# Optimization experiments

Measured on AMD Instinct MI355X. Metric: run time of the kernel, lower is better.

## Reference

```python
import jax, jax.numpy as jnp
import numpy as np
from jax import lax

B, C = 16, 80
LEVELS = [(100, 128), (50, 64), (25, 32), (13, 16), (7, 8)]
STRIDES = [8, 16, 32, 64, 128]
SCORE_THR = 0.05
IOU_THR = 0.6
MAX_DET = 1000


def make_coords(h, w, stride):
    # FCOS: center of each cell in original-image coordinates, order (x, y)
    ys = jnp.arange(h, dtype=jnp.float32) * stride + stride // 2
    xs = jnp.arange(w, dtype=jnp.float32) * stride + stride // 2
    yy, xx = jnp.meshgrid(ys, xs, indexing='ij')
    return jnp.stack([xx.reshape(-1), yy.reshape(-1)], axis=-1)  # [h*w, 2]


def flatten_levels(feats):
    # list of [B, c, h, w] -> [B, sum(h*w), c]
    return jnp.concatenate(
        [f.transpose(0, 2, 3, 1).reshape(f.shape[0], -1, f.shape[1]) for f in feats], axis=1)


def pairwise_iou(boxes):
    # boxes [N,4]; +1 area convention, matching the torch box_nms
    x1, y1, x2, y2 = boxes[:, 0], boxes[:, 1], boxes[:, 2], boxes[:, 3]
    areas = (x2 - x1 + 1.0) * (y2 - y1 + 1.0)
    xmin = jnp.maximum(x1[:, None], x1[None, :])
    ymin = jnp.maximum(y1[:, None], y1[None, :])
    xmax = jnp.minimum(x2[:, None], x2[None, :])
    ymax = jnp.minimum(y2[:, None], y2[None, :])
    inter = jnp.clip(xmax - xmin, 0.0) * jnp.clip(ymax - ymin, 0.0)
    return inter / (areas[:, None] + areas[None, :] - inter)


def nms_keep_mask(boxes, valid, thr):
    # boxes are sorted by descending score (top_k sorted=True) -> greedy order = index order
    n = boxes.shape[0]
    iou = pairwise_iou(boxes)
    idx = jnp.arange(n)

    def body(i, sup):
        kept = jnp.logical_not(sup[i])
        return sup | (kept & (iou[i] > thr) & (idx > i))

    sup = lax.fori_loop(0, n, body, jnp.logical_not(valid))
    return valid & jnp.logical_not(sup)


def detect_forward(cls_feats, ctr_feats, reg_feats):
    cls_logits = flatten_levels(cls_feats)   # [B, P, C]
    ctr_logits = flatten_levels(ctr_feats)   # [B, P, 1]
    reg_preds = flatten_levels(reg_feats)    # [B, P, 4] (l, t, r, b)
    coords = jnp.concatenate(
        [make_coords(h, w, s) for (h, w), s in zip(LEVELS, STRIDES)], axis=0)  # [P, 2]

    cls_preds = jax.nn.sigmoid(cls_logits)
    ctr_preds = jax.nn.sigmoid(ctr_logits)[..., 0]
    cls_scores = jnp.max(cls_preds, axis=-1) * ctr_preds        # add_centerness=True
    cls_classes = jnp.argmax(cls_preds, axis=-1) + 1            # [B, P] int

    boxes = jnp.concatenate(
        [coords[None] - reg_preds[..., :2], coords[None] + reg_preds[..., 2:]], axis=-1)

    max_num = min(MAX_DET, cls_scores.shape[-1])
    scores_topk, topk_ind = lax.top_k(cls_scores, max_num)      # sorted descending
    classes_topk = jnp.take_along_axis(cls_classes, topk_ind, axis=1)
    boxes_topk = jnp.take_along_axis(boxes, topk_ind[..., None], axis=1)

    valid = scores_topk >= SCORE_THR
    # batched_nms class-offset trick
    max_coord = jnp.max(boxes_topk, axis=(1, 2), keepdims=True)
    offs = classes_topk.astype(boxes_topk.dtype)[..., None] * (max_coord + 1.0)
    boxes_for_nms = boxes_topk + offs

    keep = jax.vmap(lambda b, v: nms_keep_mask(b, v, IOU_THR))(boxes_for_nms, valid)
    keep_f = keep.astype(scores_topk.dtype)
    # fixed-shape masked outputs (torch version returns ragged per-batch lists)
    return scores_topk * keep_f, classes_topk * keep, boxes_topk * keep_f[..., None]


def setup_inputs() -> dict:
    key = jax.random.key(0)
    ks = jax.random.split(key, 3 * len(LEVELS))
    inp = {}
    for i, (h, w) in enumerate(LEVELS):
        inp[f'cls{i}'] = jax.random.normal(ks[3 * i], (B, C, h, w), jnp.float32)
        inp[f'ctr{i}'] = jax.random.normal(ks[3 * i + 1], (B, 1, h, w), jnp.float32)
        # positive ltrb offsets of plausible magnitude
        inp[f'reg{i}'] = jax.random.uniform(ks[3 * i + 2], (B, 4, h, w), jnp.float32) * 64.0 + 1.0
    return inp


def reference(cls0, cls1, cls2, cls3, cls4, ctr0, ctr1, ctr2, ctr3, ctr4,
              reg0, reg1, reg2, reg3, reg4):
    return detect_forward([cls0, cls1, cls2, cls3, cls4],
                          [ctr0, ctr1, ctr2, ctr3, ctr4],
                          [reg0, reg1, reg2, reg3, reg4])
```

## Files before the change

### kernel.cpp

```cpp
#include <hip/hip_runtime.h>
#include <stdint.h>

#define NANCH 17064
#define BATCH 16
#define NCLS 80
#define KDET 1000
#define SCORE_THR 0.05f
#define IOU_THR 0.6f

typedef unsigned long long u64;
typedef unsigned int u32;

__device__ __forceinline__ float sigf(float x) { return 1.0f / (1.0f + expf(-x)); }

__device__ __forceinline__ void decode_anchor(int n, int& l, int& h, int& w) {
  if (n < 12800)      { l = 0; h = n >> 7;               w = n & 127; }
  else if (n < 16000) { l = 1; int r = n - 12800; h = r >> 6; w = r & 63; }
  else if (n < 16800) { l = 2; int r = n - 16000; h = r >> 5; w = r & 31; }
  else if (n < 17008) { l = 3; int r = n - 16800; h = r >> 4; w = r & 15; }
  else                { l = 4; int r = n - 17008; h = r >> 3; w = r & 7; }
}

__global__ __launch_bounds__(256) void k_score(
    const float* __restrict__ cls0, const float* __restrict__ ctr0,
    const float* __restrict__ cls1, const float* __restrict__ ctr1,
    const float* __restrict__ cls2, const float* __restrict__ ctr2,
    const float* __restrict__ cls3, const float* __restrict__ ctr3,
    const float* __restrict__ cls4, const float* __restrict__ ctr4,
    u32* __restrict__ sb, unsigned char* __restrict__ cl8)
{
  int n = blockIdx.x * blockDim.x + threadIdx.x;
  if (n >= NANCH) return;
  int b = blockIdx.y;
  int l, h, w; decode_anchor(n, l, h, w);
  const float* cp; const float* tp; int H, W;
  switch (l) {
    case 0: cp = cls0; tp = ctr0; H = 100; W = 128; break;
    case 1: cp = cls1; tp = ctr1; H = 50;  W = 64;  break;
    case 2: cp = cls2; tp = ctr2; H = 25;  W = 32;  break;
    case 3: cp = cls3; tp = ctr3; H = 13;  W = 16;  break;
    default: cp = cls4; tp = ctr4; H = 7;  W = 8;   break;
  }
  int hw = H * W;
  const float* base = cp + (size_t)b * NCLS * hw + h * W + w;
  float ms = -1.0f; int am = 0;
  for (int c = 0; c < NCLS; ++c) {
    float s = sigf(base[(size_t)c * hw]);
    if (s > ms) { ms = s; am = c; }
  }
  float ct = sigf(tp[(size_t)b * hw + h * W + w]);
  float score = ms * ct;
  sb[b * NANCH + n] = __float_as_uint(score);
  cl8[b * NANCH + n] = (unsigned char)am;
}

__global__ __launch_bounds__(1024) void k_topk(
    const float* __restrict__ reg0, const float* __restrict__ reg1,
    const float* __restrict__ reg2, const float* __restrict__ reg3,
    const float* __restrict__ reg4,
    const u32* __restrict__ sb, const unsigned char* __restrict__ cl8,
    float4* __restrict__ nbxG, float* __restrict__ areaG,
    float* __restrict__ scoreG, int* __restrict__ clsG, float4* __restrict__ boxG)
{
  __shared__ u32 hist[1024];
  __shared__ u32 wtot[16];
  __shared__ float wmaxS[16];
  __shared__ u64 keys[2048];
  __shared__ int s_T1, s_above, s_T2, s_cnt;

  const int tid = threadIdx.x;
  const int b = blockIdx.x;
  const int lane = tid & 63, wv = tid >> 6;
  const u32* sbb = sb + b * NANCH;

  hist[tid] = 0;
  __syncthreads();
  for (int n = tid; n < NANCH; n += 1024) atomicAdd(&hist[sbb[n] >> 22], 1u);
  __syncthreads();
  u32 h = hist[tid];
  u32 s = h;
  for (int d = 1; d < 64; d <<= 1) { u32 y = (u32)__shfl_down((int)s, d); if (lane + d < 64) s += y; }
  if (lane == 0) wtot[wv] = s;
  hist[tid] = 0;
  __syncthreads();
  {
    u32 add = 0;
    for (int w2 = wv + 1; w2 < 16; ++w2) add += wtot[w2];
    s += add;
  }
  if (s >= (u32)KDET && s - h < (u32)KDET) { s_T1 = tid; s_above = (int)(s - h); }
  __syncthreads();
  const int T1 = s_T1; const int above = s_above;

  for (int n = tid; n < NANCH; n += 1024) {
    u32 bits = sbb[n];
    if ((int)(bits >> 22) == T1) atomicAdd(&hist[(bits >> 12) & 1023u], 1u);
  }
  __syncthreads();
  h = hist[tid];
  s = h;
  for (int d = 1; d < 64; d <<= 1) { u32 y = (u32)__shfl_down((int)s, d); if (lane + d < 64) s += y; }
  if (lane == 0) wtot[wv] = s;
  __syncthreads();
  {
    u32 add = 0;
    for (int w2 = wv + 1; w2 < 16; ++w2) add += wtot[w2];
    s += add;
  }
  if (above + (int)s >= KDET && above + (int)(s - h) < KDET) s_T2 = tid;
  if (tid == 0) s_cnt = 0;
  __syncthreads();
  const int T2 = s_T2;

  for (int n = tid; n < NANCH; n += 1024) {
    u32 bits = sbb[n];
    int c1 = (int)(bits >> 22);
    bool cand = (c1 > T1) || (c1 == T1 && (int)((bits >> 12) & 1023u) >= T2);
    if (cand) {
      int pos = atomicAdd(&s_cnt, 1);
      if (pos < 2048) keys[pos] = ((u64)bits << 32) | (u64)(u32)(~(u32)n);
    }
  }
  __syncthreads();
  int C = s_cnt; if (C > 2048) C = 2048;

  float mymax = -3.4e38f;
  int posA = -1, clA = 0; float scA = 0; float4 boxA = make_float4(0, 0, 0, 0);
  int posB = -1, clB = 0; float scB = 0; float4 boxB = make_float4(0, 0, 0, 0);
  for (int t = tid; t < C; t += 1024) {
    u64 key = keys[t];
    int cnt = 0;
    for (int ss = 0; ss < C; ++ss) cnt += (keys[ss] > key) ? 1 : 0;
    if (cnt < KDET) {
      u32 bits = (u32)(key >> 32);
      int n = (int)(~(u32)(key & 0xFFFFFFFFull));
      float score = __uint_as_float(bits);
      int clsv = (int)cl8[b * NANCH + n] + 1;
      int l, hh, ww; decode_anchor(n, l, hh, ww);
      const float* rp; int W, ST, HF;
      switch (l) {
        case 0: rp = reg0; W = 128; ST = 8;   HF = 4;  break;
        case 1: rp = reg1; W = 64;  ST = 16;  HF = 8;  break;
        case 2: rp = reg2; W = 32;  ST = 32;  HF = 16; break;
        case 3: rp = reg3; W = 16;  ST = 64;  HF = 32; break;
        default: rp = reg4; W = 8;  ST = 128; HF = 64; break;
      }
      int hw; switch (l) { case 0: hw = 12800; break; case 1: hw = 3200; break;
                           case 2: hw = 800; break; case 3: hw = 208; break; default: hw = 56; }
      float cx = (float)(ww * ST + HF);
      float cy = (float)(hh * ST + HF);
      const float* rb = rp + (size_t)b * 4 * hw + hh * W + ww;
      float r0 = rb[0], r1 = rb[hw], r2 = rb[2 * hw], r3 = rb[3 * hw];
      float4 bx = make_float4(cx - r0, cy - r1, cx + r2, cy + r3);
      mymax = fmaxf(mymax, fmaxf(fmaxf(bx.x, bx.y), fmaxf(bx.z, bx.w)));
      if (posA < 0) { posA = cnt; scA = score; clA = clsv; boxA = bx; }
      else          { posB = cnt; scB = score; clB = clsv; boxB = bx; }
    }
  }

  {
    float wm = mymax;
    for (int d = 1; d < 64; d <<= 1) { float y = __shfl_down(wm, d); if (lane + d < 64) wm = fmaxf(wm, y); }
    if (lane == 0) wmaxS[wv] = wm;
  }
  __syncthreads();
  float maxc = -3.4e38f;
  for (int w2 = 0; w2 < 16; ++w2) maxc = fmaxf(maxc, wmaxS[w2]);

  if (posA >= 0) {
    int o = b * KDET + posA;
    scoreG[o] = scA; clsG[o] = clA; boxG[o] = boxA;
    float off = (float)clA * (maxc + 1.0f);
    float x1 = boxA.x + off, y1 = boxA.y + off, x2 = boxA.z + off, y2 = boxA.w + off;
    nbxG[o] = make_float4(x1, y1, x2, y2);
    areaG[o] = (x2 - x1 + 1.0f) * (y2 - y1 + 1.0f);
  }
  if (posB >= 0) {
    int o = b * KDET + posB;
    scoreG[o] = scB; clsG[o] = clB; boxG[o] = boxB;
    float off = (float)clB * (maxc + 1.0f);
    float x1 = boxB.x + off, y1 = boxB.y + off, x2 = boxB.z + off, y2 = boxB.w + off;
    nbxG[o] = make_float4(x1, y1, x2, y2);
    areaG[o] = (x2 - x1 + 1.0f) * (y2 - y1 + 1.0f);
  }
}

__global__ __launch_bounds__(256) void k_mat(
    const float4* __restrict__ nbxG, const float* __restrict__ areaG,
    u64* __restrict__ mat)
{
  __shared__ float4 nbxS[1024];
  __shared__ float areaS[1024];
  const int tid = threadIdx.x, lane = tid & 63, wv = tid >> 6;
  const int g = blockIdx.x, b = blockIdx.y;
  for (int i = tid; i < 1024; i += 256) {
    if (i < KDET) { nbxS[i] = nbxG[b * KDET + i]; areaS[i] = areaG[b * KDET + i]; }
    else          { nbxS[i] = make_float4(0, 0, 0, 0); areaS[i] = 0.0f; }
  }
  __syncthreads();
  u64* mrow = mat + (size_t)b * (KDET * 16);
  int start = g * 64, end = min(start + 64, KDET);
  for (int r = start + wv; r < end; r += 4) {
    float4 bi = nbxS[r];
    float ai = areaS[r];
    int wmax = r >> 6;
    for (int wc = 0; wc <= wmax; ++wc) {
      int j = (wc << 6) + lane;
      float4 bj = nbxS[j];
      float xmin = fmaxf(bi.x, bj.x);
      float ymin = fmaxf(bi.y, bj.y);
      float xmax = fminf(bi.z, bj.z);
      float ymax = fminf(bi.w, bj.w);
      float iw = fmaxf(xmax - xmin, 0.0f);
      float ih = fmaxf(ymax - ymin, 0.0f);
      float inter = iw * ih;
      float iou = inter / ((ai + areaS[j]) - inter);
      bool p = (j < r) && (iou > IOU_THR);
      u64 mm = __ballot(p);
      if (lane == 0) mrow[r * 16 + wc] = mm;
    }
  }
}

__global__ __launch_bounds__(1024) void k_nms(
    const u64* __restrict__ mat, const float* __restrict__ scoreG,
    const int* __restrict__ clsG, const float4* __restrict__ boxG,
    float* __restrict__ out)
{
  __shared__ u64 keptS[16];
  __shared__ int s_chg;
  const int tid = threadIdx.x;
  const int b = blockIdx.x;
  const int wv = tid >> 6, lane = tid & 63;

  float sc = (tid < KDET) ? scoreG[b * KDET + tid] : 0.0f;
  bool valid = (tid < KDET) && (sc >= SCORE_THR);

  u64 row[16];
  const u64* mrow = mat + (size_t)b * (KDET * 16) + (size_t)tid * 16;
  const int wtop = tid >> 6;
#pragma unroll
  for (int w = 0; w < 16; ++w)
    row[w] = (tid < KDET && w <= wtop) ? mrow[w] : 0ull;

  {
    u64 mb = __ballot(valid);
    if (lane == 0) keptS[wv] = mb;
  }
  __syncthreads();

  for (int it = 0; it < KDET + 1; ++it) {
    u64 sup = 0;
#pragma unroll
    for (int w = 0; w < 16; ++w) sup |= keptS[w] & row[w];
    bool nk = valid && (sup == 0ull);
    u64 nw = __ballot(nk);
    if (tid == 0) s_chg = 0;
    __syncthreads();
    if (lane == 0) {
      if (nw != keptS[wv]) s_chg = 1;
      keptS[wv] = nw;
    }
    __syncthreads();
    if (s_chg == 0) break;
  }

  if (tid < KDET) {
    bool kp = ((keptS[tid >> 6] >> (tid & 63)) & 1ull) != 0ull;
    int o1 = b * KDET + tid;
    out[o1] = kp ? sc : 0.0f;
    out[BATCH * KDET + o1] = kp ? (float)clsG[o1] : 0.0f;
    float4 bx = boxG[o1];
    float* ob = out + 2 * BATCH * KDET + (size_t)o1 * 4;
    ob[0] = kp ? bx.x : 0.0f;
    ob[1] = kp ? bx.y : 0.0f;
    ob[2] = kp ? bx.z : 0.0f;
    ob[3] = kp ? bx.w : 0.0f;
  }
}

extern "C" void kernel_launch(void* const* d_in, const int* in_sizes, int n_in,
                              void* d_out, int out_size, void* d_ws, size_t ws_size,
                              hipStream_t stream) {
  const float* cls[5]; const float* ctr[5]; const float* reg[5];
  for (int i = 0; i < 5; ++i) {
    cls[i] = (const float*)d_in[3 * i + 0];
    ctr[i] = (const float*)d_in[3 * i + 1];
    reg[i] = (const float*)d_in[3 * i + 2];
  }
  char* ws = (char*)d_ws;
  u32* sb = (u32*)ws;
  unsigned char* cl8 = (unsigned char*)(ws + 1092096);
  u64* mat = (u64*)ws;
  float4* nbxG  = (float4*)(ws + 2048000);
  float*  areaG = (float*) (ws + 2304000);
  float*  scoreG= (float*) (ws + 2368000);
  int*    clsG  = (int*)   (ws + 2432000);
  float4* boxG  = (float4*)(ws + 2496000);

  dim3 g1((NANCH + 255) / 256, BATCH);
  k_score<<<g1, 256, 0, stream>>>(cls[0], ctr[0], cls[1], ctr[1], cls[2], ctr[2],
                                  cls[3], ctr[3], cls[4], ctr[4], sb, cl8);
  k_topk<<<BATCH, 1024, 0, stream>>>(reg[0], reg[1], reg[2], reg[3], reg[4],
                                     sb, cl8, nbxG, areaG, scoreG, clsG, boxG);
  k_mat<<<dim3(16, BATCH), 256, 0, stream>>>(nbxG, areaG, mat);
  k_nms<<<BATCH, 1024, 0, stream>>>(mat, scoreG, clsG, boxG, (float*)d_out);
}
```

Before: 237.2 us.

## Split top-k ranking into multi-block kernel and tile IoU matrix per wave

The rank-by-counting step and box decoding move out of the single-block-per-image top-k kernel into a new kernel that spreads candidates across 8 blocks per image. The per-image max coordinate is reduced with an order-preserving float encoding and a global atomicMax. The IoU mask kernel now gives each wave one lower-triangular 64x64 tile, using shuffles instead of shared memory, and recomputes offset boxes inline. This trades a single serial O(C^2) loop on 16 blocks for more parallelism, at the cost of one extra launch and a global candidate buffer.

After: 201.4 us. -15.1%, faster.

```diff
diff --git a/kernel.cpp b/kernel.cpp
--- a/kernel.cpp
+++ b/kernel.cpp
@@ -19,6 +19,15 @@
   else if (n < 16800) { l = 2; int r = n - 16000; h = r >> 5; w = r & 31; }
   else if (n < 17008) { l = 3; int r = n - 16800; h = r >> 4; w = r & 15; }
   else                { l = 4; int r = n - 17008; h = r >> 3; w = r & 7; }
+}
+
+__device__ __forceinline__ u32 fenc(float f) {
+  u32 u = __float_as_uint(f);
+  return (u & 0x80000000u) ? ~u : (u | 0x80000000u);
+}
+__device__ __forceinline__ float fdec(u32 e) {
+  u32 u = (e & 0x80000000u) ? (e ^ 0x80000000u) : ~e;
+  return __uint_as_float(u);
 }
 
 __global__ __launch_bounds__(256) void k_score(
@@ -55,17 +64,11 @@
 }
 
 __global__ __launch_bounds__(1024) void k_topk(
-    const float* __restrict__ reg0, const float* __restrict__ reg1,
-    const float* __restrict__ reg2, const float* __restrict__ reg3,
-    const float* __restrict__ reg4,
-    const u32* __restrict__ sb, const unsigned char* __restrict__ cl8,
-    float4* __restrict__ nbxG, float* __restrict__ areaG,
-    float* __restrict__ scoreG, int* __restrict__ clsG, float4* __restrict__ boxG)
+    const u32* __restrict__ sb,
+    u64* __restrict__ candG, int* __restrict__ cntG, u32* __restrict__ maxcG)
 {
   __shared__ u32 hist[1024];
   __shared__ u32 wtot[16];
-  __shared__ float wmaxS[16];
-  __shared__ u64 keys[2048];
   __shared__ int s_T1, s_above, s_T2, s_cnt;
 
   const int tid = threadIdx.x;
@@ -118,108 +121,132 @@
     bool cand = (c1 > T1) || (c1 == T1 && (int)((bits >> 12) & 1023u) >= T2);
     if (cand) {
       int pos = atomicAdd(&s_cnt, 1);
-      if (pos < 2048) keys[pos] = ((u64)bits << 32) | (u64)(u32)(~(u32)n);
+      if (pos < 2048) candG[b * 2048 + pos] = ((u64)bits << 32) | (u64)(u32)(~(u32)n);
     }
   }
   __syncthreads();
-  int C = s_cnt; if (C > 2048) C = 2048;
-
-  float mymax = -3.4e38f;
-  int posA = -1, clA = 0; float scA = 0; float4 boxA = make_float4(0, 0, 0, 0);
-  int posB = -1, clB = 0; float scB = 0; float4 boxB = make_float4(0, 0, 0, 0);
-  for (int t = tid; t < C; t += 1024) {
-    u64 key = keys[t];
-    int cnt = 0;
-    for (int ss = 0; ss < C; ++ss) cnt += (keys[ss] > key) ? 1 : 0;
-    if (cnt < KDET) {
-      u32 bits = (u32)(key >> 32);
-      int n = (int)(~(u32)(key & 0xFFFFFFFFull));
-      float score = __uint_as_float(bits);
-      int clsv = (int)cl8[b * NANCH + n] + 1;
-      int l, hh, ww; decode_anchor(n, l, hh, ww);
-      const float* rp; int W, ST, HF;
-      switch (l) {
-        case 0: rp = reg0; W = 128; ST = 8;   HF = 4;  break;
-        case 1: rp = reg1; W = 64;  ST = 16;  HF = 8;  break;
-        case 2: rp = reg2; W = 32;  ST = 32;  HF = 16; break;
-        case 3: rp = reg3; W = 16;  ST = 64;  HF = 32; break;
-        default: rp = reg4; W = 8;  ST = 128; HF = 64; break;
-      }
-      int hw; switch (l) { case 0: hw = 12800; break; case 1: hw = 3200; break;
-                           case 2: hw = 800; break; case 3: hw = 208; break; default: hw = 56; }
-      float cx = (float)(ww * ST + HF);
-      float cy = (float)(hh * ST + HF);
-      const float* rb = rp + (size_t)b * 4 * hw + hh * W + ww;
-      float r0 = rb[0], r1 = rb[hw], r2 = rb[2 * hw], r3 = rb[3 * hw];
-      float4 bx = make_float4(cx - r0, cy - r1, cx + r2, cy + r3);
-      mymax = fmaxf(mymax, fmaxf(fmaxf(bx.x, bx.y), fmaxf(bx.z, bx.w)));
-      if (posA < 0) { posA = cnt; scA = score; clA = clsv; boxA = bx; }
-      else          { posB = cnt; scB = score; clB = clsv; boxB = bx; }
+  if (tid == 0) {
+    int C = s_cnt; if (C > 2048) C = 2048;
+    cntG[b] = C;
+    maxcG[b] = 0u;
+  }
+}
+
+__global__ __launch_bounds__(256) void k_rank(
+    const float* __restrict__ reg0, const float* __restrict__ reg1,
+    const float* __restrict__ reg2, const float* __restrict__ reg3,
+    const float* __restrict__ reg4,
+    const unsigned char* __restrict__ cl8,
+    const u64* __restrict__ candG, const int* __restrict__ cntG,
+    float* __restrict__ scoreG, int* __restrict__ clsG, float4* __restrict__ boxG,
+    u32* __restrict__ maxcG)
+{
+  __shared__ ulonglong2 keys2[1024];
+  const int tid = threadIdx.x;
+  const int c = blockIdx.x;
+  const int b = blockIdx.y;
+  const int lane = tid & 63;
+  const int C = cntG[b];
+  const u64* cand = candG + b * 2048;
+
+  for (int i = tid; i < 1024; i += 256) {
+    int i0 = 2 * i, i1 = 2 * i + 1;
+    ulonglong2 v;
+    v.x = (i0 < C) ? cand[i0] : 0ull;
+    v.y = (i1 < C) ? cand[i1] : 0ull;
+    keys2[i] = v;
+  }
+  __syncthreads();
+
+  const int idx = c * 256 + tid;
+  const bool active = (idx < C);
+  u64 key = active ? cand[idx] : 0ull;
+
+  int cnt = 0;
+  const int Cp2 = ((C + 7) >> 3) << 2;
+  for (int s = 0; s < Cp2; s += 4) {
+    ulonglong2 a0 = keys2[s], a1 = keys2[s + 1], a2 = keys2[s + 2], a3 = keys2[s + 3];
+    cnt += (a0.x > key) + (a0.y > key) + (a1.x > key) + (a1.y > key)
+         + (a2.x > key) + (a2.y > key) + (a3.x > key) + (a3.y > key);
+  }
+
+  u32 enc = 0u;
+  if (active && cnt < KDET) {
+    u32 bits = (u32)(key >> 32);
+    int n = (int)(~(u32)(key & 0xFFFFFFFFull));
+    float score = __uint_as_float(bits);
+    int clsv = (int)cl8[b * NANCH + n] + 1;
+    int l, hh, ww; decode_anchor(n, l, hh, ww);
+    const float* rp; int W, ST, HF, hw;
+    switch (l) {
+      case 0: rp = reg0; W = 128; ST = 8;   HF = 4;  hw = 12800; break;
+      case 1: rp = reg1; W = 64;  ST = 16;  HF = 8;  hw = 3200;  break;
+      case 2: rp = reg2; W = 32;  ST = 32;  HF = 16; hw = 800;   break;
+      case 3: rp = reg3; W = 16;  ST = 64;  HF = 32; hw = 208;   break;
+      default: rp = reg4; W = 8;  ST = 128; HF = 64; hw = 56;    break;
     }
-  }
-
-  {
-    float wm = mymax;
-    for (int d = 1; d < 64; d <<= 1) { float y = __shfl_down(wm, d); if (lane + d < 64) wm = fmaxf(wm, y); }
-    if (lane == 0) wmaxS[wv] = wm;
-  }
-  __syncthreads();
-  float maxc = -3.4e38f;
-  for (int w2 = 0; w2 < 16; ++w2) maxc = fmaxf(maxc, wmaxS[w2]);
-
-  if (posA >= 0) {
-    int o = b * KDET + posA;
-    scoreG[o] = scA; clsG[o] = clA; boxG[o] = boxA;
-    float off = (float)clA * (maxc + 1.0f);
-    float x1 = boxA.x + off, y1 = boxA.y + off, x2 = boxA.z + off, y2 = boxA.w + off;
-    nbxG[o] = make_float4(x1, y1, x2, y2);
-    areaG[o] = (x2 - x1 + 1.0f) * (y2 - y1 + 1.0f);
-  }
-  if (posB >= 0) {
-    int o = b * KDET + posB;
-    scoreG[o] = scB; clsG[o] = clB; boxG[o] = boxB;
-    float off = (float)clB * (maxc + 1.0f);
-    float x1 = boxB.x + off, y1 = boxB.y + off, x2 = boxB.z + off, y2 = boxB.w + off;
-    nbxG[o] = make_float4(x1, y1, x2, y2);
-    areaG[o] = (x2 - x1 + 1.0f) * (y2 - y1 + 1.0f);
-  }
+    float cx = (float)(ww * ST + HF);
+    float cy = (float)(hh * ST + HF);
+    const float* rb = rp + (size_t)b * 4 * hw + hh * W + ww;
+    float r0 = rb[0], r1 = rb[hw], r2 = rb[2 * hw], r3 = rb[3 * hw];
+    float4 bx = make_float4(cx - r0, cy - r1, cx + r2, cy + r3);
+    int o = b * KDET + cnt;
+    scoreG[o] = score; clsG[o] = clsv; boxG[o] = bx;
+    enc = fenc(fmaxf(fmaxf(bx.x, bx.y), fmaxf(bx.z, bx.w)));
+  }
+  for (int d = 32; d > 0; d >>= 1) {
+    u32 o = (u32)__shfl_xor((int)enc, d);
+    enc = (o > enc) ? o : enc;
+  }
+  if (lane == 0 && enc != 0u) atomicMax(maxcG + b, enc);
 }
 
 __global__ __launch_bounds__(256) void k_mat(
-    const float4* __restrict__ nbxG, const float* __restrict__ areaG,
-    u64* __restrict__ mat)
-{
-  __shared__ float4 nbxS[1024];
-  __shared__ float areaS[1024];
+    const float4* __restrict__ boxG, const int* __restrict__ clsG,
+    const u32* __restrict__ maxcG, u64* __restrict__ mat)
+{
   const int tid = threadIdx.x, lane = tid & 63, wv = tid >> 6;
-  const int g = blockIdx.x, b = blockIdx.y;
-  for (int i = tid; i < 1024; i += 256) {
-    if (i < KDET) { nbxS[i] = nbxG[b * KDET + i]; areaS[i] = areaG[b * KDET + i]; }
-    else          { nbxS[i] = make_float4(0, 0, 0, 0); areaS[i] = 0.0f; }
-  }
-  __syncthreads();
-  u64* mrow = mat + (size_t)b * (KDET * 16);
-  int start = g * 64, end = min(start + 64, KDET);
-  for (int r = start + wv; r < end; r += 4) {
-    float4 bi = nbxS[r];
-    float ai = areaS[r];
-    int wmax = r >> 6;
-    for (int wc = 0; wc <= wmax; ++wc) {
-      int j = (wc << 6) + lane;
-      float4 bj = nbxS[j];
-      float xmin = fmaxf(bi.x, bj.x);
-      float ymin = fmaxf(bi.y, bj.y);
-      float xmax = fminf(bi.z, bj.z);
-      float ymax = fminf(bi.w, bj.w);
-      float iw = fmaxf(xmax - xmin, 0.0f);
-      float ih = fmaxf(ymax - ymin, 0.0f);
-      float inter = iw * ih;
-      float iou = inter / ((ai + areaS[j]) - inter);
-      bool p = (j < r) && (iou > IOU_THR);
-      u64 mm = __ballot(p);
-      if (lane == 0) mrow[r * 16 + wc] = mm;
-    }
-  }
+  const int b = blockIdx.y;
+  const int tile = blockIdx.x * 4 + wv;
+  if (tile >= 136) return;
+  int rt = 0, rem = tile;
+  while (rem >= rt + 1) { rem -= rt + 1; ++rt; }
+  const int wc = rem;
+
+  const float scale = fdec(maxcG[b]) + 1.0f;
+
+  const int j = (wc << 6) + lane;
+  float jx1 = 0, jy1 = 0, jx2 = 0, jy2 = 0, aj = 0;
+  if (j < KDET) {
+    float4 bj = boxG[b * KDET + j];
+    float off = (float)clsG[b * KDET + j] * scale;
+    jx1 = bj.x + off; jy1 = bj.y + off; jx2 = bj.z + off; jy2 = bj.w + off;
+    aj = (jx2 - jx1 + 1.0f) * (jy2 - jy1 + 1.0f);
+  }
+  const int ri = (rt << 6) + lane;
+  float ix1 = 0, iy1 = 0, ix2 = 0, iy2 = 0;
+  if (ri < KDET) {
+    float4 bi = boxG[b * KDET + ri];
+    float off = (float)clsG[b * KDET + ri] * scale;
+    ix1 = bi.x + off; iy1 = bi.y + off; ix2 = bi.z + off; iy2 = bi.w + off;
+  }
+
+  u64 myword = 0ull;
+  for (int r = 0; r < 64; ++r) {
+    float x1 = __shfl(ix1, r), y1 = __shfl(iy1, r);
+    float x2 = __shfl(ix2, r), y2 = __shfl(iy2, r);
+    float ai = (x2 - x1 + 1.0f) * (y2 - y1 + 1.0f);
+    int row = (rt << 6) + r;
+    float xmin = fmaxf(x1, jx1), ymin = fmaxf(y1, jy1);
+    float xmax = fminf(x2, jx2), ymax = fminf(y2, jy2);
+    float inter = fmaxf(xmax - xmin, 0.0f) * fmaxf(ymax - ymin, 0.0f);
+    float iou = inter / ((ai + aj) - inter);
+    bool p = (j < row) && (j < KDET) && (iou > IOU_THR);
+    u64 mm = __ballot(p);
+    if (lane == r) myword = mm;
+  }
+  const int rowl = (rt << 6) + lane;
+  if (rowl < KDET) mat[(size_t)b * (KDET * 16) + rowl * 16 + wc] = myword;
 }
 
 __global__ __launch_bounds__(1024) void k_nms(
@@ -289,20 +316,22 @@
     reg[i] = (const float*)d_in[3 * i + 2];
   }
   char* ws = (char*)d_ws;
-  u32* sb = (u32*)ws;
+  u32* sb   = (u32*)ws;
   unsigned char* cl8 = (unsigned char*)(ws + 1092096);
-  u64* mat = (u64*)ws;
-  float4* nbxG  = (float4*)(ws + 2048000);
-  float*  areaG = (float*) (ws + 2304000);
-  float*  scoreG= (float*) (ws + 2368000);
-  int*    clsG  = (int*)   (ws + 2432000);
-  float4* boxG  = (float4*)(ws + 2496000);
+  u64* candG = (u64*)(ws + 1365120);
+  u64* mat  = (u64*)ws;
+  float*  scoreG = (float*) (ws + 2048000);
+  int*    clsG   = (int*)   (ws + 2112000);
+  float4* boxG   = (float4*)(ws + 2176000);
+  int*    cntG   = (int*)   (ws + 2432000);
+  u32*    maxcG  = (u32*)   (ws + 2432064);
 
   dim3 g1((NANCH + 255) / 256, BATCH);
   k_score<<<g1, 256, 0, stream>>>(cls[0], ctr[0], cls[1], ctr[1], cls[2], ctr[2],
                                   cls[3], ctr[3], cls[4], ctr[4], sb, cl8);
-  k_topk<<<BATCH, 1024, 0, stream>>>(reg[0], reg[1], reg[2], reg[3], reg[4],
-                                     sb, cl8, nbxG, areaG, scoreG, clsG, boxG);
-  k_mat<<<dim3(16, BATCH), 256, 0, stream>>>(nbxG, areaG, mat);
+  k_topk<<<BATCH, 1024, 0, stream>>>(sb, candG, cntG, maxcG);
+  k_rank<<<dim3(8, BATCH), 256, 0, stream>>>(reg[0], reg[1], reg[2], reg[3], reg[4],
+                                             cl8, candG, cntG, scoreG, clsG, boxG, maxcG);
+  k_mat<<<dim3(34, BATCH), 256, 0, stream>>>(boxG, clsG, maxcG, mat);
   k_nms<<<BATCH, 1024, 0, stream>>>(mat, scoreG, clsG, boxG, (float*)d_out);
 }
```
